# Kernel tuning notes

Hardware: AMD Instinct MI355X
Metric: run time of the kernel (lower is better)

The kernel has to match this reference:

```python
import jax, jax.numpy as jnp
import numpy as np

N_NEIGHBORS = 200
OUT_HW = 64

def avg_pool3(x):
    # F.avg_pool2d(x, 3, stride=1, padding=1), count_include_pad=True -> divide by 9
    s = jax.lax.reduce_window(x, 0.0, jax.lax.add, (1, 1, 3, 3), (1, 1, 1, 1),
                              ((0, 0), (0, 0), (1, 1), (1, 1)))
    return s / 9.0

def coord_conv1x1(x, w, b):
    # CoordConv2d: append normalized x/y coord channels in [-1,1], then 1x1 conv.
    B, C, H, W = x.shape
    yy = jnp.linspace(-1.0, 1.0, H, dtype=x.dtype)
    xx = jnp.linspace(-1.0, 1.0, W, dtype=x.dtype)
    xg = jnp.broadcast_to(xx[None, :], (H, W))
    yg = jnp.broadcast_to(yy[:, None], (H, W))
    coords = jnp.broadcast_to(jnp.stack([xg, yg])[None], (B, 2, H, W))
    xc = jnp.concatenate([x, coords], axis=1)  # (B, C+2, H, W)
    return jnp.einsum('bchw,oc->bohw', xc, w) + b[None, :, None, None]

def resize64(x):
    B, C, _, _ = x.shape
    return jax.image.resize(x, (B, C, OUT_HW, OUT_HW), method='bilinear')

def descriptor(p0, p1, p2, w1, b1, w2, b2, w3, b3):
    o1 = resize64(coord_conv1x1(avg_pool3(p0), w1, b1))
    o2 = resize64(coord_conv1x1(avg_pool3(p1), w2, b2))
    o3 = resize64(coord_conv1x1(avg_pool3(p2), w3, b3))
    return jnp.concatenate([o1, o2, o3], axis=1)  # (B, 1792, 64, 64)

def setup_inputs() -> dict:
    key = jax.random.key(0)
    ks = jax.random.split(key, 10)
    s = 0.05
    return {
        'p0': jax.random.normal(ks[0], (4, 256, 64, 64), jnp.float32),
        'p1': jax.random.normal(ks[1], (4, 512, 32, 32), jnp.float32),
        'p2': jax.random.normal(ks[2], (4, 1024, 16, 16), jnp.float32),
        'label': 0,
        'mask': jnp.ones((4, 1, 64, 64), jnp.float32),
        'w1': jax.random.normal(ks[3], (256, 258), jnp.float32) * s,
        'b1': jax.random.normal(ks[4], (256,), jnp.float32) * s,
        'w2': jax.random.normal(ks[5], (512, 514), jnp.float32) * s,
        'b2': jax.random.normal(ks[6], (512,), jnp.float32) * s,
        'w3': jax.random.normal(ks[7], (1024, 1026), jnp.float32) * s,
        'b3': jax.random.normal(ks[8], (1024,), jnp.float32) * s,
        'C': jax.random.normal(ks[9], (1792, 4096), jnp.float32),
    }

def reference(p0, p1, p2, label, mask, w1, b1, w2, b2, w3, b3, C):
    PHI_P = descriptor(p0, p1, p2, w1, b1, w2, b2, w3, b3)  # (B, 1792, 64, 64)
    B = PHI_P.shape[0]
    # b c h w -> b (h w) c
    phi_p = PHI_P.reshape(B, 1792, OUT_HW * OUT_HW).transpose(0, 2, 1)  # (B, 4096, 1792)
    feats = jnp.sum(phi_p * phi_p, axis=2, keepdims=True)       # (B, 4096, 1)
    cents = jnp.sum(C * C, axis=0, keepdims=True)                # (1, 4096)
    f_c = 2.0 * jnp.matmul(phi_p, C)                             # (B, 4096, 4096)
    dist = jnp.sqrt(feats + cents - f_c)
    # topk smallest: top_k on negated distances, sorted ascending after negation
    neg_vals, _ = jax.lax.top_k(-dist, N_NEIGHBORS)              # (B, 4096, 200)
    score = -neg_vals
    # b (h w) c -> b c h w
    score = score.reshape(B, OUT_HW, OUT_HW, N_NEIGHBORS).transpose(0, 3, 1, 2)
    return (score, PHI_P[:, :896, :, :])
```

## Files before the change

kernel.cpp:

```cpp
#include <hip/hip_runtime.h>
#include <hip/hip_bf16.h>
#include <stdint.h>

typedef unsigned short u16;
typedef __attribute__((ext_vector_type(8))) short bf16x8;
typedef __attribute__((ext_vector_type(4))) unsigned short u16x4;
typedef __attribute__((ext_vector_type(4))) float f32x4;

#define AS1 __attribute__((address_space(1)))
#define AS3 __attribute__((address_space(3)))

__device__ __forceinline__ u16 f2bf(float f) {
  uint32_t x = __float_as_uint(f);
  uint32_t r = (x + 0x7FFFu + ((x >> 16) & 1u)) >> 16;
  return (u16)r;
}
__device__ __forceinline__ float bf2f(u16 u) {
  return __uint_as_float(((uint32_t)u) << 16);
}

__device__ __forceinline__ void gload_lds16(const void* g, void* l) {
  __builtin_amdgcn_global_load_lds((const AS1 void*)g, (AS3 void*)l, 16, 0, 0);
}

template <int C, int H, int W>
__global__ __launch_bounds__(256) void pool_trans(const float* __restrict__ in,
                                                  u16* __restrict__ PT) {
  constexpr int HW = H * W;
  int hwt = blockIdx.x, ct = blockIdx.y, b = blockIdx.z;
  int tid = threadIdx.x;
  __shared__ float t[32][33];
  {
    int c_l = tid >> 3;
    int hw_l = (tid & 7) * 4;
    int c = ct * 32 + c_l;
    int hw = hwt * 32 + hw_l;
    int y = hw / W;
    int x0 = hw % W;
    const float* pl = in + ((size_t)b * C + c) * HW;
    float cs[6] = {0, 0, 0, 0, 0, 0};
    #pragma unroll
    for (int dy = -1; dy <= 1; dy++) {
      int yy = y + dy;
      if ((unsigned)yy < (unsigned)H) {
        const float* row = pl + yy * W;
        #pragma unroll
        for (int k = 0; k < 6; k++) {
          int xx = x0 - 1 + k;
          if ((unsigned)xx < (unsigned)W) cs[k] += row[xx];
        }
      }
    }
    #pragma unroll
    for (int k = 0; k < 4; k++)
      t[c_l][hw_l + k] = (cs[k] + cs[k + 1] + cs[k + 2]) * (1.0f / 9.0f);
  }
  __syncthreads();
  int hw_w = tid >> 3;
  int c_w = (tid & 7) * 4;
  u16x4 o;
  #pragma unroll
  for (int j = 0; j < 4; j++) o[j] = f2bf(t[c_w + j][hw_w]);
  *(u16x4*)&PT[((size_t)b * HW + hwt * 32 + hw_w) * C + ct * 32 + c_w] = o;
}

__global__ void wconv_bf16(const float* __restrict__ wf, u16* __restrict__ wb,
                           int logk, int total) {
  int idx = blockIdx.x * 256 + threadIdx.x;
  if (idx >= total) return;
  int K = 1 << logk;
  int o = idx >> (logk - 3);
  int k0 = (idx & ((K >> 3) - 1)) * 8;
  const float* src = wf + (size_t)o * (K + 2) + k0;
  bf16x8 v;
  #pragma unroll
  for (int e = 0; e < 8; e++) v[e] = (short)f2bf(src[e]);
  *(bf16x8*)&wb[(size_t)o * K + k0] = v;
}

template <int K, int HW, int WD, int OC, int PHIC, int CST>
__global__ __launch_bounds__(256) void conv_gemm(
    const u16* __restrict__ Wb,
    const u16* __restrict__ PT,
    const float* __restrict__ wf,
    const float* __restrict__ bias,
    float* __restrict__ outHW, size_t outHW_bstride,
    u16* __restrict__ outCM) {
  constexpr int LOGW = (WD == 64) ? 6 : (WD == 32) ? 5 : 4;
  constexpr int LOGHW = 2 * LOGW;
  int n0 = blockIdx.x * 128, m0 = blockIdx.y * 128;
  int tid = threadIdx.x;
  int wid = tid >> 6, lane = tid & 63;
  int wm = wid >> 1, wn = wid & 1;
  __shared__ u16 As[128 * 64];
  __shared__ u16 Bs[128 * 64];
  f32x4 acc[4][4] = {};
  int lrow = tid >> 3;
  int lcol = (tid & 7) * 8;
  const u16* ga = Wb + (size_t)(m0 + lrow) * K + lcol;
  const u16* gb = PT + (size_t)(n0 + lrow) * K + lcol;
  char* lbaseA = (char*)As + wid * 1024;
  char* lbaseB = (char*)Bs + wid * 1024;
  for (int k0 = 0; k0 < K; k0 += 64) {
    #pragma unroll
    for (int q = 0; q < 4; q++) {
      gload_lds16(ga + (size_t)q * 32 * K + k0, lbaseA + q * 4096);
      gload_lds16(gb + (size_t)q * 32 * K + k0, lbaseB + q * 4096);
    }
    __syncthreads();
    #pragma unroll
    for (int kk = 0; kk < 2; kk++) {
      bf16x8 af[4], bfr[4];
      int kb = kk * 32 + (lane >> 4) * 8;
      #pragma unroll
      for (int i = 0; i < 4; i++)
        af[i] = *(const bf16x8*)&As[(wm * 64 + i * 16 + (lane & 15)) * 64 + kb];
      #pragma unroll
      for (int j = 0; j < 4; j++)
        bfr[j] = *(const bf16x8*)&Bs[(wn * 64 + j * 16 + (lane & 15)) * 64 + kb];
      #pragma unroll
      for (int i = 0; i < 4; i++)
        #pragma unroll
        for (int j = 0; j < 4; j++)
          acc[i][j] = __builtin_amdgcn_mfma_f32_16x16x32_bf16(af[i], bfr[j], acc[i][j], 0, 0, 0);
    }
    __syncthreads();
  }
  int rq = lane >> 4, cq = lane & 15;
  #pragma unroll
  for (int mi = 0; mi < 4; mi++) {
    int lm = m0 + wm * 64 + mi * 16 + rq * 4;
    float wxr[4], wyr[4], bbr[4];
    #pragma unroll
    for (int r = 0; r < 4; r++) {
      int o = lm + r;
      wxr[r] = wf[(size_t)o * (K + 2) + K];
      wyr[r] = wf[(size_t)o * (K + 2) + K + 1];
      bbr[r] = bias[o];
    }
    #pragma unroll
    for (int ni = 0; ni < 4; ni++) {
      int gn = n0 + wn * 64 + ni * 16 + cq;
      int b = gn >> LOGHW;
      int hw = gn & (HW - 1);
      int x = hw & (WD - 1), y = hw >> LOGW;
      float xg = -1.0f + x * (2.0f / (WD - 1));
      float yg = -1.0f + y * (2.0f / (WD - 1));
      float vals[4];
      #pragma unroll
      for (int r = 0; r < 4; r++)
        vals[r] = acc[mi][ni][r] + wxr[r] * xg + wyr[r] * yg + bbr[r];
      if (lm < PHIC) {
        #pragma unroll
        for (int r = 0; r < 4; r++)
          outHW[(size_t)b * outHW_bstride + (size_t)(lm + r) * HW + hw] = vals[r];
      }
      u16x4 pk;
      #pragma unroll
      for (int r = 0; r < 4; r++) pk[r] = f2bf(vals[r]);
      *(u16x4*)&outCM[((size_t)b * HW + hw) * CST + lm] = pk;
    }
  }
}

template <int Hin>
__device__ __forceinline__ void bilin_coords(int v, int& i0, int& i1, float& wgt) {
  constexpr float scale = (float)Hin / 64.0f;
  float f = ((float)v + 0.5f) * scale - 0.5f;
  float f0 = floorf(f);
  wgt = f - f0;
  int i = (int)f0;
  i1 = min(i + 1, Hin - 1);
  i0 = max(i, 0);
}

template <int C, int Cin, int Hin>
__global__ void emit_phi_v(const float* __restrict__ in, float* __restrict__ outp,
                           int ch_off) {
  int idx = blockIdx.x * 256 + threadIdx.x;
  int x0 = (idx & 15) * 4;
  int y = (idx >> 4) & 63;
  int c = (idx >> 10) % C;
  int b = idx / (C * 1024);
  const float* pl = in + (size_t)(b * Cin + c) * (Hin * Hin);
  int y0, y1; float wy;
  bilin_coords<Hin>(y, y0, y1, wy);
  const float* r0 = pl + y0 * Hin;
  const float* r1 = pl + y1 * Hin;
  f32x4 o;
  #pragma unroll
  for (int k = 0; k < 4; k++) {
    int xx0, xx1; float wx;
    bilin_coords<Hin>(x0 + k, xx0, xx1, wx);
    float top = (1.0f - wx) * r0[xx0] + wx * r0[xx1];
    float bot = (1.0f - wx) * r1[xx0] + wx * r1[xx1];
    o[k] = (1.0f - wy) * top + wy * bot;
  }
  *(f32x4*)&outp[((size_t)b * 896 + ch_off + c) * 4096 + (y << 6) + x0] = o;
}

__global__ __launch_bounds__(256) void trans_f32_bf16(
    const float* __restrict__ in, u16* __restrict__ outT, int R, int Cc, int OS,
    size_t in_bstride, size_t out_bstride) {
  int b = blockIdx.z;
  in += (size_t)b * in_bstride;
  outT += (size_t)b * out_bstride;
  int r0 = blockIdx.y * 32, c0 = blockIdx.x * 32;
  __shared__ float t[32][33];
  int tid = threadIdx.x;
  int cl = tid & 31, rl = tid >> 5;
  #pragma unroll
  for (int q = 0; q < 4; q++)
    t[rl + q * 8][cl] = in[(size_t)(r0 + rl + q * 8) * Cc + c0 + cl];
  __syncthreads();
  #pragma unroll
  for (int q = 0; q < 4; q++) {
    int c = c0 + rl + q * 8;
    outT[(size_t)c * OS + r0 + cl] = f2bf(t[cl][rl + q * 8]);
  }
}

template <int C, int Hin, int L>
__global__ void gather_A(const u16* __restrict__ OT, u16* __restrict__ A,
                         int ch_off) {
  int idx = blockIdx.x * 256 + threadIdx.x;
  int co = (idx & ((C / 8) - 1)) * 8;
  int hw = (idx >> L) & 4095;
  int b = idx >> (L + 12);
  int x = hw & 63, y = hw >> 6;
  int y0, y1, x0, x1; float wy, wx;
  bilin_coords<Hin>(y, y0, y1, wy);
  bilin_coords<Hin>(x, x0, x1, wx);
  float w00 = (1.0f - wy) * (1.0f - wx), w01 = (1.0f - wy) * wx;
  float w10 = wy * (1.0f - wx), w11 = wy * wx;
  const u16* base = OT + (size_t)b * (Hin * Hin) * C + co;
  bf16x8 t00 = *(const bf16x8*)&base[(y0 * Hin + x0) * C];
  bf16x8 t01 = *(const bf16x8*)&base[(y0 * Hin + x1) * C];
  bf16x8 t10 = *(const bf16x8*)&base[(y1 * Hin + x0) * C];
  bf16x8 t11 = *(const bf16x8*)&base[(y1 * Hin + x1) * C];
  bf16x8 o;
  #pragma unroll
  for (int e = 0; e < 8; e++) {
    float v = w00 * bf2f((u16)t00[e]) + w01 * bf2f((u16)t01[e]) +
              w10 * bf2f((u16)t10[e]) + w11 * bf2f((u16)t11[e]);
    o[e] = (short)f2bf(v);
  }
  *(bf16x8*)&A[((size_t)b * 4096 + hw) * 1792 + ch_off + co] = o;
}

__global__ __launch_bounds__(256) void rownorm2(const u16* __restrict__ X,
                                                float* __restrict__ out, int ncols) {
  int row = blockIdx.x * 4 + (threadIdx.x >> 6);
  int lane = threadIdx.x & 63;
  const u16* xr = X + (size_t)row * ncols;
  int n8 = ncols >> 3;
  float s = 0.0f;
  for (int c8 = lane; c8 < n8; c8 += 64) {
    bf16x8 v = *(const bf16x8*)&xr[c8 * 8];
    #pragma unroll
    for (int e = 0; e < 8; e++) {
      float f = bf2f((u16)v[e]);
      s = fmaf(f, f, s);
    }
  }
  #pragma unroll
  for (int off = 32; off; off >>= 1) s += __shfl_down(s, off);
  if (lane == 0) out[row] = s;
}

#define GD_NT 56

__device__ __forceinline__ void stage16k(const u16* __restrict__ G, int row0,
                                         int k0, char* lds_wavebase, int lane) {
  const int K = 1792;
  int sub = lane >> 2;
  int colsw = 8 * ((lane & 3) ^ ((lane >> 3) & 3));
  #pragma unroll
  for (int q = 0; q < 2; q++) {
    gload_lds16(G + (size_t)(row0 + q * 128 + sub) * K + k0 + colsw,
                lds_wavebase + q * 8192);
  }
}

__global__ __launch_bounds__(512, 2) void gemm_dist2(
    const u16* __restrict__ A,
    const u16* __restrict__ Bt,
    const float* __restrict__ feats, const float* __restrict__ cents,
    u16* __restrict__ S16, int m_base) {
  const int K = 1792, N = 4096;
  extern __shared__ u16 lds[];
  int bid = blockIdx.x;
  int swz = (bid & 7) * 32 + (bid >> 3);
  int m0 = (swz >> 4) * 256;
  int n0 = (swz & 15) * 256;
  int tid = threadIdx.x;
  int wid = tid >> 6, lane = tid & 63;
  int wr = wid >> 2, wc = wid & 3;
  int ln15 = lane & 15;
  int fo = 8 * ((lane >> 4) ^ ((lane >> 1) & 3));

  f32x4 acc[8][4] = {};

  #pragma unroll
  for (int t = 0; t < 3; t++) {
    char* bufb = (char*)lds + (t & 3) * 32768 + wid * 1024;
    stage16k(A, m_base + m0 + wid * 16, t * 32, bufb, lane);
    stage16k(Bt, n0 + wid * 16, t * 32, bufb + 16384, lane);
  }

  #pragma unroll 1
  for (int t = 0; t < GD_NT; t++) {
    asm volatile("s_waitcnt vmcnt(8)" ::: "memory");
    __builtin_amdgcn_s_barrier();
    __builtin_amdgcn_sched_barrier(0);
    const u16* Ab = lds + (t & 3) * 16384;
    const u16* Bb = Ab + 8192;
    char* nbuf = (char*)lds + ((t + 3) & 3) * 32768 + wid * 1024;

    bf16x8 bq[4], af[8];
    #pragma unroll
    for (int ni = 0; ni < 4; ni++)
      bq[ni] = *(const bf16x8*)&Bb[(wc * 64 + ni * 16 + ln15) * 32 + fo];
    #pragma unroll
    for (int mi = 0; mi < 8; mi++)
      af[mi] = *(const bf16x8*)&Ab[(wr * 128 + mi * 16 + ln15) * 32 + fo];

    if (t + 3 < GD_NT) {
      stage16k(A, m_base + m0 + wid * 16, (t + 3) * 32, nbuf, lane);
      stage16k(Bt, n0 + wid * 16, (t + 3) * 32, nbuf + 16384, lane);
    }

    __builtin_amdgcn_s_setprio(1);
    #pragma unroll
    for (int mi = 0; mi < 8; mi++)
      #pragma unroll
      for (int ni = 0; ni < 4; ni++)
        acc[mi][ni] = __builtin_amdgcn_mfma_f32_16x16x32_bf16(af[mi], bq[ni], acc[mi][ni], 0, 0, 0);
    __builtin_amdgcn_s_setprio(0);
  }

  int rq = lane >> 4, cq = lane & 15;
  #pragma unroll
  for (int mi = 0; mi < 8; mi++) {
    int lm = m0 + wr * 128 + mi * 16 + rq * 4;
    #pragma unroll
    for (int ni = 0; ni < 4; ni++) {
      int gn = n0 + wc * 64 + ni * 16 + cq;
      float cn = cents[gn];
      #pragma unroll
      for (int r = 0; r < 4; r++)
        S16[(size_t)(lm + r) * N + gn] =
            f2bf(feats[m_base + lm + r] + cn - 2.0f * acc[mi][ni][r]);
    }
  }
}

__global__ __launch_bounds__(256) void select_topk(const u16* __restrict__ S16,
                                                   float* __restrict__ out,
                                                   int row_base) {
  int wv = threadIdx.x >> 6, lane = threadIdx.x & 63;
  int row_local = blockIdx.x * 4 + wv;
  const u16* Sr = S16 + (size_t)row_local * 4096;
  uint32_t ku[64];
  #pragma unroll
  for (int g = 0; g < 8; g++) {
    bf16x8 v = *(const bf16x8*)&Sr[g * 512 + lane * 8];
    #pragma unroll
    for (int e = 0; e < 8; e++) {
      uint32_t u = (uint32_t)(u16)v[e];
      u ^= (u & 0x8000u) ? 0xFFFFu : 0x8000u;
      ku[g * 8 + e] = u;
    }
  }
  uint32_t mn = 0xFFFFu, mx = 0u;
  #pragma unroll
  for (int j = 0; j < 64; j++) {
    mn = min(mn, ku[j]);
    mx = max(mx, ku[j]);
  }
  #pragma unroll
  for (int off = 1; off < 64; off <<= 1) {
    mn = min(mn, (uint32_t)__shfl_xor((int)mn, off));
    mx = max(mx, (uint32_t)__shfl_xor((int)mx, off));
  }
  uint32_t lo = mn, hi = mx;
  while (lo < hi) {
    uint32_t mid = (lo + hi) >> 1;
    int c = 0;
    #pragma unroll
    for (int j = 0; j < 64; j++) c += (ku[j] <= mid) ? 1 : 0;
    #pragma unroll
    for (int off = 1; off < 64; off <<= 1) c += __shfl_xor(c, off);
    if (c >= 200) hi = mid; else lo = mid + 1;
  }
  uint32_t T = lo;
  int cl = 0;
  #pragma unroll
  for (int j = 0; j < 64; j++) cl += (ku[j] < T) ? 1 : 0;
  int incl = cl;
  #pragma unroll
  for (int off = 1; off < 64; off <<= 1) {
    int v = __shfl_up(incl, off);
    if (lane >= off) incl += v;
  }
  int nless = __shfl(incl, 63);
  int pos = incl - cl;
  __shared__ uint32_t selv[4][256];
  uint32_t* sv = selv[wv];
  #pragma unroll
  for (int g = 0; g < 4; g++) sv[g * 64 + lane] = 0xFFFFFFFFu;
  for (int p = nless + lane; p < 200; p += 64) sv[p] = T;
  #pragma unroll
  for (int j = 0; j < 64; j++)
    if (ku[j] < T) sv[pos++] = ku[j];
  uint32_t v[4];
  #pragma unroll
  for (int q = 0; q < 4; q++) v[q] = sv[q * 64 + lane];
  #pragma unroll
  for (int kk = 2; kk <= 256; kk <<= 1) {
    #pragma unroll
    for (int jj = kk >> 1; jj > 0; jj >>= 1) {
      if (jj >= 64) {
        int qb = jj >> 6;
        #pragma unroll
        for (int q = 0; q < 4; q++) {
          if ((q & qb) == 0) {
            int q2 = q | qb;
            bool up = (kk == 256) ? true : ((q & (kk >> 6)) == 0);
            uint32_t a = v[q], b2 = v[q2];
            uint32_t lo2 = min(a, b2), hi2 = max(a, b2);
            v[q] = up ? lo2 : hi2;
            v[q2] = up ? hi2 : lo2;
          }
        }
      } else {
        #pragma unroll
        for (int q = 0; q < 4; q++) {
          bool up;
          if (kk == 256) up = true;
          else if (kk == 128) up = ((q & 2) == 0);
          else if (kk == 64) up = ((q & 1) == 0);
          else up = ((lane & kk) == 0);
          uint32_t other = (uint32_t)__shfl_xor((int)v[q], jj);
          bool lower = ((lane & jj) == 0);
          uint32_t lo2 = min(v[q], other), hi2 = max(v[q], other);
          v[q] = (up == lower) ? lo2 : hi2;
        }
      }
    }
  }
  int grow = row_base + row_local;
  int b = grow >> 12, r = grow & 4095;
  #pragma unroll
  for (int q = 0; q < 4; q++) {
    int i = q * 64 + lane;
    if (i < 200) {
      uint32_t u = v[q] & 0xFFFFu;
      u ^= (u & 0x8000u) ? 0x8000u : 0xFFFFu;
      out[((size_t)b * 200 + i) * 4096 + r] = sqrtf(bf2f((u16)u));
    }
  }
}

extern "C" void kernel_launch(void* const* d_in, const int* in_sizes, int n_in,
                              void* d_out, int out_size, void* d_ws, size_t ws_size,
                              hipStream_t stream) {
  const float* p0 = (const float*)d_in[0];
  const float* p1 = (const float*)d_in[1];
  const float* p2 = (const float*)d_in[2];
  const float* w1 = (const float*)d_in[5];
  const float* b1 = (const float*)d_in[6];
  const float* w2 = (const float*)d_in[7];
  const float* b2 = (const float*)d_in[8];
  const float* w3 = (const float*)d_in[9];
  const float* b3 = (const float*)d_in[10];
  const float* Cm = (const float*)d_in[11];

  float* out_score = (float*)d_out;
  float* out_phi = (float*)d_out + 3276800;

  char* w = (char*)d_ws;
  u16* Abf = (u16*)w;
  u16* Ct = (u16*)(w + 58720256);
  float* feats = (float*)(w + 73400320);
  float* cents = (float*)(w + 73465856);
  u16* S16 = (u16*)(w + 73482240);
  u16* PT1 = (u16*)(w + 73482240);
  u16* PT2 = (u16*)(w + 81870848);
  u16* PT3 = (u16*)(w + 86065152);
  u16* Wbf1 = (u16*)(w + 88162304);
  u16* Wbf2 = (u16*)(w + 88293376);
  u16* Wbf3 = (u16*)(w + 88817664);
  float* O2 = (float*)(w + 90914816);
  float* O3 = (float*)(w + 99303424);
  u16* OT2 = (u16*)(w + 99827712);
  u16* OT3 = (u16*)(w + 104022016);

  pool_trans<256, 64, 64><<<dim3(128, 8, 4), 256, 0, stream>>>(p0, PT1);
  pool_trans<512, 32, 32><<<dim3(32, 16, 4), 256, 0, stream>>>(p1, PT2);
  pool_trans<1024, 16, 16><<<dim3(8, 32, 4), 256, 0, stream>>>(p2, PT3);

  wconv_bf16<<<32, 256, 0, stream>>>(w1, Wbf1, 8, 8192);
  wconv_bf16<<<128, 256, 0, stream>>>(w2, Wbf2, 9, 32768);
  wconv_bf16<<<512, 256, 0, stream>>>(w3, Wbf3, 10, 131072);

  conv_gemm<256, 4096, 64, 256, 256, 1792><<<dim3(128, 2), 256, 0, stream>>>(
      Wbf1, PT1, w1, b1, out_phi, (size_t)896 * 4096, Abf);
  conv_gemm<512, 1024, 32, 512, 512, 512><<<dim3(32, 4), 256, 0, stream>>>(
      Wbf2, PT2, w2, b2, O2, (size_t)512 * 1024, OT2);
  conv_gemm<1024, 256, 16, 1024, 128, 1024><<<dim3(8, 8), 256, 0, stream>>>(
      Wbf3, PT3, w3, b3, O3, (size_t)128 * 256, OT3);

  emit_phi_v<512, 512, 32><<<8192, 256, 0, stream>>>(O2, out_phi, 256);
  emit_phi_v<128, 128, 16><<<2048, 256, 0, stream>>>(O3, out_phi, 768);

  gather_A<512, 32, 6><<<4096, 256, 0, stream>>>(OT2, Abf, 256);
  gather_A<1024, 16, 7><<<8192, 256, 0, stream>>>(OT3, Abf, 768);

  trans_f32_bf16<<<dim3(128, 56, 1), 256, 0, stream>>>(Cm, Ct, 1792, 4096, 1792, 0, 0);

  rownorm2<<<4096, 256, 0, stream>>>(Abf, feats, 1792);
  rownorm2<<<1024, 256, 0, stream>>>(Ct, cents, 1792);

  for (int mc = 0; mc < 4; mc++) {
    gemm_dist2<<<256, 512, 131072, stream>>>(Abf, Ct, feats, cents, S16, mc * 4096);
    select_topk<<<1024, 256, 0, stream>>>(S16, out_score, mc * 4096);
  }
}
```

Baseline: 460.5 us.

## Switch distance GEMM operands and staging to FP8 e4m3 MFMA

Converts the descriptor matrix A and the transposed centroid matrix to FP8 e4m3 instead of bf16, and runs the distance GEMM with 16x16x32 fp8 MFMA. This halves operand bytes, LDS staging per tile and dynamic shared memory. The staging and fragment-offset swizzles are reworked for 8-bit elements, and the row norms are computed from the fp8 values. FP8 quantization of unnormalized features risks large errors in the distances and in the top-k ordering.

Measured after the change: 466.8 us. Within noise of the previous version (+1.4%).

```diff
diff --git a/kernel.cpp b/kernel.cpp
--- a/kernel.cpp
+++ b/kernel.cpp
@@ -1,5 +1,6 @@
 #include <hip/hip_runtime.h>
 #include <hip/hip_bf16.h>
+#include <hip/hip_fp8.h>
 #include <stdint.h>
 
 typedef unsigned short u16;
@@ -17,6 +18,15 @@
 }
 __device__ __forceinline__ float bf2f(u16 u) {
   return __uint_as_float(((uint32_t)u) << 16);
+}
+__device__ __forceinline__ uint8_t f2f8(float f) {
+  __hip_fp8_e4m3 t(f);
+  return (uint8_t)t.__x;
+}
+__device__ __forceinline__ float f82f(uint8_t v) {
+  __hip_fp8_e4m3 t;
+  t.__x = (__hip_fp8_storage_t)v;
+  return (float)t;
 }
 
 __device__ __forceinline__ void gload_lds16(const void* g, void* l) {
@@ -78,14 +88,14 @@
   *(bf16x8*)&wb[(size_t)o * K + k0] = v;
 }
 
-template <int K, int HW, int WD, int OC, int PHIC, int CST>
+template <int K, int HW, int WD, int OC, int PHIC, int CST, bool OUT8>
 __global__ __launch_bounds__(256) void conv_gemm(
     const u16* __restrict__ Wb,
     const u16* __restrict__ PT,
     const float* __restrict__ wf,
     const float* __restrict__ bias,
     float* __restrict__ outHW, size_t outHW_bstride,
-    u16* __restrict__ outCM) {
+    void* __restrict__ outCM) {
   constexpr int LOGW = (WD == 64) ? 6 : (WD == 32) ? 5 : 4;
   constexpr int LOGHW = 2 * LOGW;
   int n0 = blockIdx.x * 128, m0 = blockIdx.y * 128;
@@ -155,10 +165,16 @@
         for (int r = 0; r < 4; r++)
           outHW[(size_t)b * outHW_bstride + (size_t)(lm + r) * HW + hw] = vals[r];
       }
-      u16x4 pk;
-      #pragma unroll
-      for (int r = 0; r < 4; r++) pk[r] = f2bf(vals[r]);
-      *(u16x4*)&outCM[((size_t)b * HW + hw) * CST + lm] = pk;
+      if constexpr (OUT8) {
+        uint32_t pk = (uint32_t)f2f8(vals[0]) | ((uint32_t)f2f8(vals[1]) << 8) |
+                      ((uint32_t)f2f8(vals[2]) << 16) | ((uint32_t)f2f8(vals[3]) << 24);
+        *(uint32_t*)&((uint8_t*)outCM)[((size_t)b * HW + hw) * CST + lm] = pk;
+      } else {
+        u16x4 pk;
+        #pragma unroll
+        for (int r = 0; r < 4; r++) pk[r] = f2bf(vals[r]);
+        *(u16x4*)&((u16*)outCM)[((size_t)b * HW + hw) * CST + lm] = pk;
+      }
     }
   }
 }
@@ -199,12 +215,8 @@
   *(f32x4*)&outp[((size_t)b * 896 + ch_off + c) * 4096 + (y << 6) + x0] = o;
 }
 
-__global__ __launch_bounds__(256) void trans_f32_bf16(
-    const float* __restrict__ in, u16* __restrict__ outT, int R, int Cc, int OS,
-    size_t in_bstride, size_t out_bstride) {
-  int b = blockIdx.z;
-  in += (size_t)b * in_bstride;
-  outT += (size_t)b * out_bstride;
+__global__ __launch_bounds__(256) void trans_f32_fp8(
+    const float* __restrict__ in, uint8_t* __restrict__ outT, int R, int Cc, int OS) {
   int r0 = blockIdx.y * 32, c0 = blockIdx.x * 32;
   __shared__ float t[32][33];
   int tid = threadIdx.x;
@@ -216,12 +228,12 @@
   #pragma unroll
   for (int q = 0; q < 4; q++) {
     int c = c0 + rl + q * 8;
-    outT[(size_t)c * OS + r0 + cl] = f2bf(t[cl][rl + q * 8]);
+    outT[(size_t)c * OS + r0 + cl] = f2f8(t[cl][rl + q * 8]);
   }
 }
 
 template <int C, int Hin, int L>
-__global__ void gather_A(const u16* __restrict__ OT, u16* __restrict__ A,
+__global__ void gather_A(const u16* __restrict__ OT, uint8_t* __restrict__ A,
                          int ch_off) {
   int idx = blockIdx.x * 256 + threadIdx.x;
   int co = (idx & ((C / 8) - 1)) * 8;
@@ -238,28 +250,34 @@
   bf16x8 t01 = *(const bf16x8*)&base[(y0 * Hin + x1) * C];
   bf16x8 t10 = *(const bf16x8*)&base[(y1 * Hin + x0) * C];
   bf16x8 t11 = *(const bf16x8*)&base[(y1 * Hin + x1) * C];
-  bf16x8 o;
+  uint32_t pk[2] = {0, 0};
   #pragma unroll
   for (int e = 0; e < 8; e++) {
     float v = w00 * bf2f((u16)t00[e]) + w01 * bf2f((u16)t01[e]) +
               w10 * bf2f((u16)t10[e]) + w11 * bf2f((u16)t11[e]);
-    o[e] = (short)f2bf(v);
-  }
-  *(bf16x8*)&A[((size_t)b * 4096 + hw) * 1792 + ch_off + co] = o;
-}
-
-__global__ __launch_bounds__(256) void rownorm2(const u16* __restrict__ X,
+    pk[e >> 2] |= ((uint32_t)f2f8(v)) << ((e & 3) * 8);
+  }
+  uint2 o; o.x = pk[0]; o.y = pk[1];
+  *(uint2*)&A[((size_t)b * 4096 + hw) * 1792 + ch_off + co] = o;
+}
+
+__global__ __launch_bounds__(256) void rownorm8(const uint8_t* __restrict__ X,
                                                 float* __restrict__ out, int ncols) {
   int row = blockIdx.x * 4 + (threadIdx.x >> 6);
   int lane = threadIdx.x & 63;
-  const u16* xr = X + (size_t)row * ncols;
+  const uint8_t* xr = X + (size_t)row * ncols;
   int n8 = ncols >> 3;
   float s = 0.0f;
   for (int c8 = lane; c8 < n8; c8 += 64) {
-    bf16x8 v = *(const bf16x8*)&xr[c8 * 8];
-    #pragma unroll
-    for (int e = 0; e < 8; e++) {
-      float f = bf2f((u16)v[e]);
+    uint2 v = *(const uint2*)&xr[c8 * 8];
+    #pragma unroll
+    for (int e = 0; e < 4; e++) {
+      float f = f82f((uint8_t)((v.x >> (8 * e)) & 0xFF));
+      s = fmaf(f, f, s);
+    }
+    #pragma unroll
+    for (int e = 0; e < 4; e++) {
+      float f = f82f((uint8_t)((v.y >> (8 * e)) & 0xFF));
       s = fmaf(f, f, s);
     }
   }
@@ -270,25 +288,21 @@
 
 #define GD_NT 56
 
-__device__ __forceinline__ void stage16k(const u16* __restrict__ G, int row0,
-                                         int k0, char* lds_wavebase, int lane) {
+__device__ __forceinline__ void stage8k(const uint8_t* __restrict__ G, int row0,
+                                        int k0, char* lds_wavebase, int lane) {
   const int K = 1792;
-  int sub = lane >> 2;
-  int colsw = 8 * ((lane & 3) ^ ((lane >> 3) & 3));
-  #pragma unroll
-  for (int q = 0; q < 2; q++) {
-    gload_lds16(G + (size_t)(row0 + q * 128 + sub) * K + k0 + colsw,
-                lds_wavebase + q * 8192);
-  }
+  int r = lane >> 1;
+  int h = (lane & 1) ^ ((lane >> 3) & 1);
+  gload_lds16(G + (size_t)(row0 + r) * K + k0 + h * 16, lds_wavebase);
 }
 
 __global__ __launch_bounds__(512, 2) void gemm_dist2(
-    const u16* __restrict__ A,
-    const u16* __restrict__ Bt,
+    const uint8_t* __restrict__ A,
+    const uint8_t* __restrict__ Bt,
     const float* __restrict__ feats, const float* __restrict__ cents,
     u16* __restrict__ S16, int m_base) {
   const int K = 1792, N = 4096;
-  extern __shared__ u16 lds[];
+  extern __shared__ uint8_t lds8[];
   int bid = blockIdx.x;
   int swz = (bid & 7) * 32 + (bid >> 3);
   int m0 = (swz >> 4) * 256;
@@ -297,37 +311,38 @@
   int wid = tid >> 6, lane = tid & 63;
   int wr = wid >> 2, wc = wid & 3;
   int ln15 = lane & 15;
-  int fo = 8 * ((lane >> 4) ^ ((lane >> 1) & 3));
+  int key = (ln15 >> 2) & 1;
+  int fo8 = (((lane >> 5) ^ key) << 4) | (((lane >> 4) & 1) << 3);
 
   f32x4 acc[8][4] = {};
 
   #pragma unroll
   for (int t = 0; t < 3; t++) {
-    char* bufb = (char*)lds + (t & 3) * 32768 + wid * 1024;
-    stage16k(A, m_base + m0 + wid * 16, t * 32, bufb, lane);
-    stage16k(Bt, n0 + wid * 16, t * 32, bufb + 16384, lane);
+    char* bufb = (char*)lds8 + (t & 3) * 16384 + wid * 1024;
+    stage8k(A, m_base + m0 + wid * 32, t * 32, bufb, lane);
+    stage8k(Bt, n0 + wid * 32, t * 32, bufb + 8192, lane);
   }
 
   #pragma unroll 1
   for (int t = 0; t < GD_NT; t++) {
-    asm volatile("s_waitcnt vmcnt(8)" ::: "memory");
+    asm volatile("s_waitcnt vmcnt(4)" ::: "memory");
     __builtin_amdgcn_s_barrier();
     __builtin_amdgcn_sched_barrier(0);
-    const u16* Ab = lds + (t & 3) * 16384;
-    const u16* Bb = Ab + 8192;
-    char* nbuf = (char*)lds + ((t + 3) & 3) * 32768 + wid * 1024;
-
-    bf16x8 bq[4], af[8];
+    const uint8_t* Ab = lds8 + (t & 3) * 16384;
+    const uint8_t* Bb = Ab + 8192;
+    char* nbuf = (char*)lds8 + ((t + 3) & 3) * 16384 + wid * 1024;
+
+    long bq[4], af[8];
     #pragma unroll
     for (int ni = 0; ni < 4; ni++)
-      bq[ni] = *(const bf16x8*)&Bb[(wc * 64 + ni * 16 + ln15) * 32 + fo];
+      bq[ni] = *(const long*)&Bb[(wc * 64 + ni * 16 + ln15) * 32 + fo8];
     #pragma unroll
     for (int mi = 0; mi < 8; mi++)
-      af[mi] = *(const bf16x8*)&Ab[(wr * 128 + mi * 16 + ln15) * 32 + fo];
+      af[mi] = *(const long*)&Ab[(wr * 128 + mi * 16 + ln15) * 32 + fo8];
 
     if (t + 3 < GD_NT) {
-      stage16k(A, m_base + m0 + wid * 16, (t + 3) * 32, nbuf, lane);
-      stage16k(Bt, n0 + wid * 16, (t + 3) * 32, nbuf + 16384, lane);
+      stage8k(A, m_base + m0 + wid * 32, (t + 3) * 32, nbuf, lane);
+      stage8k(Bt, n0 + wid * 32, (t + 3) * 32, nbuf + 8192, lane);
     }
 
     __builtin_amdgcn_s_setprio(1);
@@ -335,7 +350,7 @@
     for (int mi = 0; mi < 8; mi++)
       #pragma unroll
       for (int ni = 0; ni < 4; ni++)
-        acc[mi][ni] = __builtin_amdgcn_mfma_f32_16x16x32_bf16(af[mi], bq[ni], acc[mi][ni], 0, 0, 0);
+        acc[mi][ni] = __builtin_amdgcn_mfma_f32_16x16x32_fp8_fp8(af[mi], bq[ni], acc[mi][ni], 0, 0, 0);
     __builtin_amdgcn_s_setprio(0);
   }
 
@@ -480,21 +495,21 @@
   float* out_phi = (float*)d_out + 3276800;
 
   char* w = (char*)d_ws;
-  u16* Abf = (u16*)w;
-  u16* Ct = (u16*)(w + 58720256);
-  float* feats = (float*)(w + 73400320);
-  float* cents = (float*)(w + 73465856);
-  u16* S16 = (u16*)(w + 73482240);
-  u16* PT1 = (u16*)(w + 73482240);
-  u16* PT2 = (u16*)(w + 81870848);
-  u16* PT3 = (u16*)(w + 86065152);
-  u16* Wbf1 = (u16*)(w + 88162304);
-  u16* Wbf2 = (u16*)(w + 88293376);
-  u16* Wbf3 = (u16*)(w + 88817664);
-  float* O2 = (float*)(w + 90914816);
-  float* O3 = (float*)(w + 99303424);
-  u16* OT2 = (u16*)(w + 99827712);
-  u16* OT3 = (u16*)(w + 104022016);
+  uint8_t* A8 = (uint8_t*)w;
+  uint8_t* Ct8 = (uint8_t*)(w + 29360128);
+  float* feats = (float*)(w + 36700160);
+  float* cents = (float*)(w + 36765696);
+  u16* S16 = (u16*)(w + 36782080);
+  u16* PT1 = (u16*)(w + 36782080);
+  u16* PT2 = (u16*)(w + 45170688);
+  u16* PT3 = (u16*)(w + 49364992);
+  u16* Wbf1 = (u16*)(w + 51462144);
+  u16* Wbf2 = (u16*)(w + 51593216);
+  u16* Wbf3 = (u16*)(w + 52117504);
+  float* O2 = (float*)(w + 54214656);
+  float* O3 = (float*)(w + 62603264);
+  u16* OT2 = (u16*)(w + 63127552);
+  u16* OT3 = (u16*)(w + 67321856);
 
   pool_trans<256, 64, 64><<<dim3(128, 8, 4), 256, 0, stream>>>(p0, PT1);
   pool_trans<512, 32, 32><<<dim3(32, 16, 4), 256, 0, stream>>>(p1, PT2);
@@ -504,26 +519,26 @@
   wconv_bf16<<<128, 256, 0, stream>>>(w2, Wbf2, 9, 32768);
   wconv_bf16<<<512, 256, 0, stream>>>(w3, Wbf3, 10, 131072);
 
-  conv_gemm<256, 4096, 64, 256, 256, 1792><<<dim3(128, 2), 256, 0, stream>>>(
-      Wbf1, PT1, w1, b1, out_phi, (size_t)896 * 4096, Abf);
-  conv_gemm<512, 1024, 32, 512, 512, 512><<<dim3(32, 4), 256, 0, stream>>>(
+  conv_gemm<256, 4096, 64, 256, 256, 1792, true><<<dim3(128, 2), 256, 0, stream>>>(
+      Wbf1, PT1, w1, b1, out_phi, (size_t)896 * 4096, A8);
+  conv_gemm<512, 1024, 32, 512, 512, 512, false><<<dim3(32, 4), 256, 0, stream>>>(
       Wbf2, PT2, w2, b2, O2, (size_t)512 * 1024, OT2);
-  conv_gemm<1024, 256, 16, 1024, 128, 1024><<<dim3(8, 8), 256, 0, stream>>>(
+  conv_gemm<1024, 256, 16, 1024, 128, 1024, false><<<dim3(8, 8), 256, 0, stream>>>(
       Wbf3, PT3, w3, b3, O3, (size_t)128 * 256, OT3);
 
   emit_phi_v<512, 512, 32><<<8192, 256, 0, stream>>>(O2, out_phi, 256);
   emit_phi_v<128, 128, 16><<<2048, 256, 0, stream>>>(O3, out_phi, 768);
 
-  gather_A<512, 32, 6><<<4096, 256, 0, stream>>>(OT2, Abf, 256);
-  gather_A<1024, 16, 7><<<8192, 256, 0, stream>>>(OT3, Abf, 768);
-
-  trans_f32_bf16<<<dim3(128, 56, 1), 256, 0, stream>>>(Cm, Ct, 1792, 4096, 1792, 0, 0);
-
-  rownorm2<<<4096, 256, 0, stream>>>(Abf, feats, 1792);
-  rownorm2<<<1024, 256, 0, stream>>>(Ct, cents, 1792);
+  gather_A<512, 32, 6><<<4096, 256, 0, stream>>>(OT2, A8, 256);
+  gather_A<1024, 16, 7><<<8192, 256, 0, stream>>>(OT3, A8, 768);
+
+  trans_f32_fp8<<<dim3(128, 56), 256, 0, stream>>>(Cm, Ct8, 1792, 4096, 1792);
+
+  rownorm8<<<4096, 256, 0, stream>>>(A8, feats, 1792);
+  rownorm8<<<1024, 256, 0, stream>>>(Ct8, cents, 1792);
 
   for (int mc = 0; mc < 4; mc++) {
-    gemm_dist2<<<256, 512, 131072, stream>>>(Abf, Ct, feats, cents, S16, mc * 4096);
+    gemm_dist2<<<256, 512, 65536, stream>>>(A8, Ct8, feats, cents, S16, mc * 4096);
     select_topk<<<1024, 256, 0, stream>>>(S16, out_score, mc * 4096);
   }
 }
```
